# Kernel optimization log

Measured on AMD Instinct MI355X. Metric: run time of the kernel, lower is better.

The kernel has to match this reference:

```python
import jax, jax.numpy as jnp
import numpy as np

NUM_USERS = 100000
NUM_ITEMS = 50000
N_NODES = NUM_USERS + NUM_ITEMS
EMB = 64          # emb_dim == layers[0]
NNZ = 2_400_000   # ~16 avg degree normalized-Laplacian nonzeros
BATCH = 16384


def spmm(rows, cols, vals, x, n):
    # sparse (COO) Laplacian @ dense features: out[r] += v * x[c]
    return jax.ops.segment_sum(vals[:, None] * x[cols], rows, num_segments=n)


def setup_inputs() -> dict:
    key = jax.random.key(0)
    ks = jax.random.split(key, 20)
    userIdx = jax.random.randint(ks[0], (BATCH,), 0, NUM_USERS)
    itemIdx = jax.random.randint(ks[1], (BATCH,), 0, NUM_ITEMS)
    lap_rows = jax.random.randint(ks[2], (NNZ,), 0, N_NODES, dtype=jnp.int32)
    lap_cols = jax.random.randint(ks[3], (NNZ,), 0, N_NODES, dtype=jnp.int32)
    # normalized Laplacian values ~ 1/sqrt(deg_i*deg_j), small positive
    lap_vals = jax.random.uniform(ks[4], (NNZ,), dtype=jnp.float32) * 0.05
    uEmb = jax.random.normal(ks[5], (NUM_USERS, EMB), dtype=jnp.float32) * 0.1
    iEmb = jax.random.normal(ks[6], (NUM_ITEMS, EMB), dtype=jnp.float32) * 0.1
    s = 1.0 / np.sqrt(EMB)
    gW0 = jax.random.normal(ks[7], (EMB, EMB), dtype=jnp.float32) * s
    gb0 = jnp.zeros((EMB,), jnp.float32)
    gW1 = jax.random.normal(ks[8], (EMB, EMB), dtype=jnp.float32) * s
    gb1 = jnp.zeros((EMB,), jnp.float32)
    D_CAT = EMB * 3 * 2  # 384
    W1 = jax.random.normal(ks[9], (D_CAT, 64), dtype=jnp.float32) / np.sqrt(D_CAT)
    b1 = jnp.zeros((64,), jnp.float32)
    W2 = jax.random.normal(ks[10], (64, 32), dtype=jnp.float32) / 8.0
    b2 = jnp.zeros((32,), jnp.float32)
    W3 = jax.random.normal(ks[11], (32, 1), dtype=jnp.float32) / np.sqrt(32.0)
    b3 = jnp.zeros((1,), jnp.float32)
    return {"userIdx": userIdx, "itemIdx": itemIdx,
            "lap_rows": lap_rows, "lap_cols": lap_cols, "lap_vals": lap_vals,
            "uEmb": uEmb, "iEmb": iEmb,
            "gW0": gW0, "gb0": gb0, "gW1": gW1, "gb1": gb1,
            "W1": W1, "b1": b1, "W2": W2, "b2": b2, "W3": W3, "b3": b3}


def reference(userIdx, itemIdx, lap_rows, lap_cols, lap_vals,
              uEmb, iEmb, gW0, gb0, gW1, gb1, W1, b1, W2, b2, W3, b3):
    features = jnp.concatenate([uEmb, iEmb], axis=0)  # [N, EMB]
    final = features
    for W, b in ((gW0, gb0), (gW1, gb1)):
        # (Laplacian + selfLoop I) @ features, then linear + ReLU
        h = spmm(lap_rows, lap_cols, lap_vals, features, N_NODES) + features
        features = jax.nn.relu(h @ W + b)
        final = jnp.concatenate([final, features], axis=1)
    u = final[userIdx]                     # [B, 192]
    it = final[itemIdx + NUM_USERS]        # [B, 192]
    e = jnp.concatenate([u, it], axis=1)   # [B, 384]
    e = jax.nn.relu(e @ W1 + b1)
    e = e @ W2 + b2
    e = e @ W3 + b3
    return e.ravel()
```

## Files before the change

### kernel.cpp

```cpp
#include <hip/hip_runtime.h>
#include <hip/hip_bf16.h>

#define NUM_USERS 100000
#define NUM_ITEMS 50000
#define N_NODES   150000
#define EMB       64
#define NNZ       2400000
#define BATCH     16384
#define D_CAT     384
#define BSHIFT    8
#define NBUCK     ((N_NODES + 255) >> 8)
#define EPB       9375

__device__ __forceinline__ unsigned short f2bf(float f) {
    unsigned u = __float_as_uint(f);
    unsigned r = u + 0x7fffu + ((u >> 16) & 1u);
    return (unsigned short)(r >> 16);
}
__device__ __forceinline__ float bflo(unsigned u) { return __uint_as_float(u << 16); }
__device__ __forceinline__ float bfhi(unsigned u) { return __uint_as_float(u & 0xffff0000u); }

__global__ __launch_bounds__(1024) void bucket_hist(const int* __restrict__ rows,
                                                    int* __restrict__ bcnt, int nnz) {
    __shared__ int h[NBUCK];
    int tid = threadIdx.x;
    for (int i = tid; i < NBUCK; i += 1024) h[i] = 0;
    __syncthreads();
    for (int i = blockIdx.x * 1024 + tid; i < nnz; i += gridDim.x * 1024)
        atomicAdd(&h[rows[i] >> BSHIFT], 1);
    __syncthreads();
    for (int i = tid; i < NBUCK; i += 1024) {
        int c = h[i];
        if (c) atomicAdd(&bcnt[i], c);
    }
}

__global__ __launch_bounds__(1024) void bucket_scan(const int* __restrict__ bcnt,
                                                    int* __restrict__ boffs,
                                                    int* __restrict__ gtails, int nnz) {
    __shared__ int s[1024];
    int t = threadIdx.x;
    int x = (t < NBUCK) ? bcnt[t] : 0;
    s[t] = x;
    __syncthreads();
#pragma unroll
    for (int off = 1; off < 1024; off <<= 1) {
        int v = (t >= off) ? s[t - off] : 0;
        __syncthreads();
        s[t] += v;
        __syncthreads();
    }
    if (t < NBUCK) {
        int e = s[t] - x;
        boffs[t] = e;
        gtails[t] = e;
    }
    if (t == 0) boffs[NBUCK] = nnz;
}

__global__ __launch_bounds__(1024) void coarse_multisplit(const int* __restrict__ rows,
                                                          const int* __restrict__ cols,
                                                          const float* __restrict__ vals,
                                                          int* __restrict__ gtails,
                                                          int2* __restrict__ pv, int nnz) {
    extern __shared__ int dyn[];
    int2* stage = (int2*)dyn;
    int*  smap  = dyn + 2 * EPB;
    __shared__ int hcnt[NBUCK];
    __shared__ int lstart[NBUCK];
    __shared__ int shiftv[NBUCK];

    int tid = threadIdx.x;
    int e0 = blockIdx.x * EPB;
    int e1 = e0 + EPB < nnz ? e0 + EPB : nnz;
    int nE = e1 - e0;

    for (int i = tid; i < NBUCK; i += 1024) hcnt[i] = 0;
    __syncthreads();
    for (int i = e0 + tid; i < e1; i += 1024)
        atomicAdd(&hcnt[rows[i] >> BSHIFT], 1);
    __syncthreads();

    int cnt = (tid < NBUCK) ? hcnt[tid] : 0;
    smap[tid] = cnt;
    __syncthreads();
#pragma unroll
    for (int off = 1; off < 1024; off <<= 1) {
        int v = (tid >= off) ? smap[tid - off] : 0;
        __syncthreads();
        smap[tid] += v;
        __syncthreads();
    }
    if (tid < NBUCK) {
        int ls = smap[tid] - cnt;
        lstart[tid] = ls;
        hcnt[tid] = ls;
        int gb = cnt ? atomicAdd(&gtails[tid], cnt) : 0;
        shiftv[tid] = gb - ls;
    }
    __syncthreads();

    for (int b = tid; b < NBUCK; b += 1024) {
        int beg = lstart[b];
        int end_ = (b == NBUCK - 1) ? nE : lstart[b + 1];
        int sh = shiftv[b];
        for (int k = beg; k < end_; ++k) smap[k] = sh;
    }
    __syncthreads();

    for (int i = e0 + tid; i < e1; i += 1024) {
        int r = rows[i];
        int p = atomicAdd(&hcnt[r >> BSHIFT], 1);
        stage[p] = make_int2(((r & 255) << 18) | cols[i], __float_as_int(vals[i]));
    }
    __syncthreads();

    for (int j = tid; j < nE; j += 1024)
        pv[smap[j] + j] = stage[j];
}

__global__ __launch_bounds__(1024) void fine_scatter(const int* __restrict__ boffs,
                                                     const int2* __restrict__ pv,
                                                     int2* __restrict__ packed,
                                                     int* __restrict__ row_ptr, int nnz) {
    __shared__ int rcnt[256];
    __shared__ int loff[256];
    int b = blockIdx.x;
    int tid = threadIdx.x;
    int lo = boffs[b], hi = boffs[b + 1];
    int r0 = b << BSHIFT;
    int nr = N_NODES - r0; if (nr > 256) nr = 256;

    if (tid < 256) rcnt[tid] = 0;
    __syncthreads();
    for (int i = lo + tid; i < hi; i += 1024)
        atomicAdd(&rcnt[pv[i].x >> 18], 1);
    __syncthreads();
    if (tid < 256) loff[tid] = rcnt[tid];
    __syncthreads();
#pragma unroll
    for (int off = 1; off < 256; off <<= 1) {
        int v = (tid < 256 && tid >= off) ? loff[tid - off] : 0;
        __syncthreads();
        if (tid < 256) loff[tid] += v;
        __syncthreads();
    }
    if (tid < 256) {
        int e = lo + loff[tid] - rcnt[tid];
        loff[tid] = e;
        if (tid < nr) row_ptr[r0 + tid] = e;
    }
    if (b == 0 && tid == 0) row_ptr[N_NODES] = nnz;
    __syncthreads();
    for (int i = lo + tid; i < hi; i += 1024) {
        int2 e = pv[i];
        int rl = e.x >> 18;
        int pos = atomicAdd(&loff[rl], 1);
        packed[pos] = make_int2(e.x & 0x3FFFF, e.y);
    }
}

__global__ __launch_bounds__(256) void gemm_table_f32(const float* __restrict__ uE,
                                                      const float* __restrict__ iE,
                                                      const float* __restrict__ W,
                                                      unsigned short* __restrict__ Zh,
                                                      int n_rows) {
    __shared__ float Wl[64 * 64];
    __shared__ float Xf[64 * 64];
    int tid = threadIdx.x;
    int lane = tid & 63;
    int wave = tid >> 6;
    int r0 = blockIdx.x * 64;
    int last = n_rows - 1;

    for (int i = tid; i < 64 * 64; i += 256) Wl[i] = W[i];
    for (int i = tid; i < 64 * 16; i += 256) {
        int row = i >> 4, q = i & 15;
        int r = r0 + row; r = r > last ? last : r;
        const float4* src = (r < NUM_USERS)
            ? (const float4*)(uE + (size_t)r * 64)
            : (const float4*)(iE + (size_t)(r - NUM_USERS) * 64);
        ((float4*)Xf)[i] = src[q];
    }
    __syncthreads();

    int rbase = wave * 16;
    float acc[16];
#pragma unroll
    for (int i = 0; i < 16; ++i) acc[i] = 0.f;

#pragma unroll 1
    for (int kc = 0; kc < 16; ++kc) {
        float w0 = Wl[(kc * 4 + 0) * 64 + lane];
        float w1 = Wl[(kc * 4 + 1) * 64 + lane];
        float w2 = Wl[(kc * 4 + 2) * 64 + lane];
        float w3 = Wl[(kc * 4 + 3) * 64 + lane];
#pragma unroll
        for (int i = 0; i < 16; ++i) {
            float4 q = ((const float4*)Xf)[(rbase + i) * 16 + kc];
            acc[i] = fmaf(q.x, w0, acc[i]);
            acc[i] = fmaf(q.y, w1, acc[i]);
            acc[i] = fmaf(q.z, w2, acc[i]);
            acc[i] = fmaf(q.w, w3, acc[i]);
        }
    }
#pragma unroll
    for (int i = 0; i < 16; ++i) {
        int r = r0 + rbase + i;
        if (r < n_rows) Zh[(size_t)r * 64 + lane] = f2bf(acc[i]);
    }
}

__global__ __launch_bounds__(256) void gemm_table_bf16(const unsigned* __restrict__ Xh,
                                                       const float* __restrict__ W,
                                                       unsigned short* __restrict__ Zh,
                                                       int n_rows) {
    __shared__ float Wl[64 * 64];
    __shared__ uint4 Xl4[64 * 8];
    int tid = threadIdx.x;
    int lane = tid & 63;
    int wave = tid >> 6;
    int r0 = blockIdx.x * 64;
    int nr = n_rows - r0; if (nr > 64) nr = 64;

    for (int i = tid; i < 64 * 64; i += 256) Wl[i] = W[i];
    const uint4* Xg4 = (const uint4*)(Xh + (size_t)r0 * 32);
    for (int i = tid; i < nr * 8; i += 256) Xl4[i] = Xg4[i];
    __syncthreads();

    const unsigned* Xl = (const unsigned*)Xl4;
    int rbase = wave * 16;
    float acc[16];
#pragma unroll
    for (int i = 0; i < 16; ++i) acc[i] = 0.f;

#pragma unroll 1
    for (int kc = 0; kc < 8; ++kc) {
        float w0 = Wl[(kc * 8 + 0) * 64 + lane];
        float w1 = Wl[(kc * 8 + 1) * 64 + lane];
        float w2 = Wl[(kc * 8 + 2) * 64 + lane];
        float w3 = Wl[(kc * 8 + 3) * 64 + lane];
        float w4 = Wl[(kc * 8 + 4) * 64 + lane];
        float w5 = Wl[(kc * 8 + 5) * 64 + lane];
        float w6 = Wl[(kc * 8 + 6) * 64 + lane];
        float w7 = Wl[(kc * 8 + 7) * 64 + lane];
#pragma unroll
        for (int i = 0; i < 16; ++i) {
            uint4 q = *(const uint4*)&Xl[(rbase + i) * 32 + kc * 4];
            acc[i] = fmaf(bflo(q.x), w0, acc[i]);
            acc[i] = fmaf(bfhi(q.x), w1, acc[i]);
            acc[i] = fmaf(bflo(q.y), w2, acc[i]);
            acc[i] = fmaf(bfhi(q.y), w3, acc[i]);
            acc[i] = fmaf(bflo(q.z), w4, acc[i]);
            acc[i] = fmaf(bfhi(q.z), w5, acc[i]);
            acc[i] = fmaf(bflo(q.w), w6, acc[i]);
            acc[i] = fmaf(bfhi(q.w), w7, acc[i]);
        }
    }
#pragma unroll
    for (int i = 0; i < 16; ++i) {
        int r = r0 + rbase + i;
        if (r < n_rows) Zh[(size_t)r * 64 + lane] = f2bf(acc[i]);
    }
}

__global__ __launch_bounds__(256) void spmm_bias_relu(const int* __restrict__ row_ptr,
                                                      const int2* __restrict__ packed,
                                                      const uint2* __restrict__ zh2,
                                                      const float* __restrict__ bias,
                                                      uint2* __restrict__ outh2,
                                                      int n_rows) {
    int tid = threadIdx.x;
    int lane = tid & 63;
    int wave = tid >> 6;
    int q = lane >> 4;
    int k = lane & 15;
    int r = blockIdx.x * 4 + wave;
    if (r >= n_rows) return;

    uint2 su = zh2[(size_t)r * 16 + k];
    float4 acc;
    acc.x = q ? 0.f : bflo(su.x);
    acc.y = q ? 0.f : bfhi(su.x);
    acc.z = q ? 0.f : bflo(su.y);
    acc.w = q ? 0.f : bfhi(su.y);

    int e = row_ptr[r] + q;
    int end = row_ptr[r + 1];
    for (; e + 13 < end; e += 16) {
        int2 p0 = packed[e + 0];
        int2 p1 = packed[e + 4];
        int2 p2 = packed[e + 8];
        int2 p3 = packed[e + 12];
        uint2 z0 = zh2[(size_t)p0.x * 16 + k];
        uint2 z1 = zh2[(size_t)p1.x * 16 + k];
        uint2 z2 = zh2[(size_t)p2.x * 16 + k];
        uint2 z3 = zh2[(size_t)p3.x * 16 + k];
        float v0 = __int_as_float(p0.y), v1 = __int_as_float(p1.y);
        float v2 = __int_as_float(p2.y), v3 = __int_as_float(p3.y);
        acc.x = fmaf(v0, bflo(z0.x), acc.x); acc.y = fmaf(v0, bfhi(z0.x), acc.y);
        acc.z = fmaf(v0, bflo(z0.y), acc.z); acc.w = fmaf(v0, bfhi(z0.y), acc.w);
        acc.x = fmaf(v1, bflo(z1.x), acc.x); acc.y = fmaf(v1, bfhi(z1.x), acc.y);
        acc.z = fmaf(v1, bflo(z1.y), acc.z); acc.w = fmaf(v1, bfhi(z1.y), acc.w);
        acc.x = fmaf(v2, bflo(z2.x), acc.x); acc.y = fmaf(v2, bfhi(z2.x), acc.y);
        acc.z = fmaf(v2, bflo(z2.y), acc.z); acc.w = fmaf(v2, bfhi(z2.y), acc.w);
        acc.x = fmaf(v3, bflo(z3.x), acc.x); acc.y = fmaf(v3, bfhi(z3.x), acc.y);
        acc.z = fmaf(v3, bflo(z3.y), acc.z); acc.w = fmaf(v3, bfhi(z3.y), acc.w);
    }
    for (; e < end; e += 4) {
        int2 p = packed[e];
        uint2 z = zh2[(size_t)p.x * 16 + k];
        float v = __int_as_float(p.y);
        acc.x = fmaf(v, bflo(z.x), acc.x); acc.y = fmaf(v, bfhi(z.x), acc.y);
        acc.z = fmaf(v, bflo(z.y), acc.z); acc.w = fmaf(v, bfhi(z.y), acc.w);
    }

    acc.x += __shfl_xor(acc.x, 16, 64);
    acc.y += __shfl_xor(acc.y, 16, 64);
    acc.z += __shfl_xor(acc.z, 16, 64);
    acc.w += __shfl_xor(acc.w, 16, 64);
    acc.x += __shfl_xor(acc.x, 32, 64);
    acc.y += __shfl_xor(acc.y, 32, 64);
    acc.z += __shfl_xor(acc.z, 32, 64);
    acc.w += __shfl_xor(acc.w, 32, 64);
    if (q == 0) {
        float4 bv = ((const float4*)bias)[k];
        float a = fmaxf(acc.x + bv.x, 0.f);
        float b = fmaxf(acc.y + bv.y, 0.f);
        float c = fmaxf(acc.z + bv.z, 0.f);
        float d = fmaxf(acc.w + bv.w, 0.f);
        outh2[(size_t)r * 16 + k] = make_uint2(
            ((unsigned)f2bf(b) << 16) | (unsigned)f2bf(a),
            ((unsigned)f2bf(d) << 16) | (unsigned)f2bf(c));
    }
}

__global__ __launch_bounds__(1024) void fused_mlp(
        const int* __restrict__ userIdx, const int* __restrict__ itemIdx,
        const float* __restrict__ uEmb, const float* __restrict__ iEmb,
        const unsigned short* __restrict__ feat1h,
        const unsigned short* __restrict__ feat2h,
        const float* __restrict__ W1, const float* __restrict__ b1,
        const float* __restrict__ W2, const float* __restrict__ b2,
        const float* __restrict__ W3, const float* __restrict__ b3,
        float* __restrict__ out) {
    __shared__ float    Wl[128 * 64];
    __shared__ unsigned El[64 * 64];
    __shared__ float    Ht[64 * 64];
    __shared__ float    W2l[64 * 32];
    __shared__ float    w3l[32];
    __shared__ float    b2l[32];
    __shared__ int      uidx[64], iidx[64];
    int tid = threadIdx.x;
    int lane = tid & 63;
    int wave = tid >> 6;
    int r0 = blockIdx.x * 64;
    int rbase = wave * 4;

    if (tid < 64) uidx[tid] = userIdx[r0 + tid];
    else if (tid < 128) iidx[tid - 64] = itemIdx[r0 + tid - 64];
    if (tid < 32) { w3l[tid] = W3[tid]; b2l[tid] = b2[tid]; }
    for (int i = tid; i < 64 * 32; i += 1024) W2l[i] = W2[i];

    float acc[4];
    float bv = b1[lane];
#pragma unroll
    for (int i = 0; i < 4; ++i) acc[i] = bv;

#pragma unroll 1
    for (int c = 0; c < 3; ++c) {
        __syncthreads();
        for (int i = tid; i < 128 * 64; i += 1024) Wl[i] = W1[c * 128 * 64 + i];
        {
            int t = tid;
            int row = t >> 4;
            int seg = (t >> 3) & 1;
            int q   = t & 7;
            int gseg = c * 2 + seg;
            uint4 val;
            if (gseg == 0 || gseg == 3) {
                const float* p = (gseg == 0)
                    ? uEmb + (size_t)uidx[row] * 64 + q * 8
                    : iEmb + (size_t)iidx[row] * 64 + q * 8;
                float4 a = *(const float4*)p;
                float4 b = *(const float4*)(p + 4);
                val.x = ((unsigned)f2bf(a.y) << 16) | f2bf(a.x);
                val.y = ((unsigned)f2bf(a.w) << 16) | f2bf(a.z);
                val.z = ((unsigned)f2bf(b.y) << 16) | f2bf(b.x);
                val.w = ((unsigned)f2bf(b.w) << 16) | f2bf(b.z);
            } else {
                const unsigned short* src;
                if (gseg == 1)      src = feat1h + (size_t)uidx[row] * 64;
                else if (gseg == 2) src = feat2h + (size_t)uidx[row] * 64;
                else if (gseg == 4) src = feat1h + (size_t)(iidx[row] + NUM_USERS) * 64;
                else                src = feat2h + (size_t)(iidx[row] + NUM_USERS) * 64;
                val = *(const uint4*)(src + q * 8);
            }
            *(uint4*)&El[row * 64 + seg * 32 + q * 4] = val;
        }
        __syncthreads();
        const uint4* El4 = (const uint4*)El;
#pragma unroll 1
        for (int k = 0; k < 128; k += 8) {
            float w0 = Wl[(k + 0) * 64 + lane];
            float w1 = Wl[(k + 1) * 64 + lane];
            float w2 = Wl[(k + 2) * 64 + lane];
            float w3 = Wl[(k + 3) * 64 + lane];
            float w4 = Wl[(k + 4) * 64 + lane];
            float w5 = Wl[(k + 5) * 64 + lane];
            float w6 = Wl[(k + 6) * 64 + lane];
            float w7 = Wl[(k + 7) * 64 + lane];
#pragma unroll
            for (int i = 0; i < 4; ++i) {
                uint4 q = El4[(rbase + i) * 16 + (k >> 3)];
                acc[i] = fmaf(bflo(q.x), w0, acc[i]);
                acc[i] = fmaf(bfhi(q.x), w1, acc[i]);
                acc[i] = fmaf(bflo(q.y), w2, acc[i]);
                acc[i] = fmaf(bfhi(q.y), w3, acc[i]);
                acc[i] = fmaf(bflo(q.z), w4, acc[i]);
                acc[i] = fmaf(bfhi(q.z), w5, acc[i]);
                acc[i] = fmaf(bflo(q.w), w6, acc[i]);
                acc[i] = fmaf(bfhi(q.w), w7, acc[i]);
            }
        }
    }

#pragma unroll
    for (int i = 0; i < 4; ++i) Ht[(rbase + i) * 64 + lane] = fmaxf(acc[i], 0.f);
    __syncthreads();

    int half = lane >> 5;
    int k = lane & 31;
    float b3v = b3[0];
#pragma unroll 1
    for (int p = 0; p < 2; ++p) {
        int row = rbase + p * 2 + half;
        float z = b2l[k];
#pragma unroll
        for (int j = 0; j < 64; ++j)
            z = fmaf(Ht[row * 64 + j], W2l[j * 32 + k], z);
        z *= w3l[k];
#pragma unroll
        for (int off = 16; off; off >>= 1)
            z += __shfl_xor(z, off, 64);
        if (k == 0) out[r0 + row] = z + b3v;
    }
}

extern "C" void kernel_launch(void* const* d_in, const int* in_sizes, int n_in,
                              void* d_out, int out_size, void* d_ws, size_t ws_size,
                              hipStream_t stream) {
    const int*   userIdx = (const int*)  d_in[0];
    const int*   itemIdx = (const int*)  d_in[1];
    const int*   lap_rows= (const int*)  d_in[2];
    const int*   lap_cols= (const int*)  d_in[3];
    const float* lap_vals= (const float*)d_in[4];
    const float* uEmb    = (const float*)d_in[5];
    const float* iEmb    = (const float*)d_in[6];
    const float* gW0     = (const float*)d_in[7];
    const float* gb0     = (const float*)d_in[8];
    const float* gW1     = (const float*)d_in[9];
    const float* gb1     = (const float*)d_in[10];
    const float* W1      = (const float*)d_in[11];
    const float* b1      = (const float*)d_in[12];
    const float* W2      = (const float*)d_in[13];
    const float* b2      = (const float*)d_in[14];
    const float* W3      = (const float*)d_in[15];
    const float* b3      = (const float*)d_in[16];
    float* out = (float*)d_out;

    const size_t NF = (size_t)N_NODES * EMB;
    char* w = (char*)d_ws;
    unsigned short* bufA = (unsigned short*)w;
    unsigned short* bufB = bufA + NF;
    char*  region3 = (char*)(bufB + NF);
    int2*  pv      = (int2*)region3;
    unsigned short* Zh = (unsigned short*)region3;
    int2*  packed  = (int2*)(region3 + NF * sizeof(float));
    int*   row_ptr = (int*)(packed + NNZ);
    int*   boffs   = row_ptr + (N_NODES + 1);
    int*   gtails  = boffs + (NBUCK + 1);
    int*   bcnt    = gtails + NBUCK;

    const int ms_grid   = (NNZ + EPB - 1) / EPB;
    const int ms_lds    = EPB * 12;
    const int spmm_grid = (N_NODES + 3) / 4;
    const int gemm_grid = (N_NODES + 63) / 64;

    hipMemsetAsync(bcnt, 0, NBUCK * sizeof(int), stream);
    bucket_hist<<<256, 1024, 0, stream>>>(lap_rows, bcnt, NNZ);
    bucket_scan<<<1, 1024, 0, stream>>>(bcnt, boffs, gtails, NNZ);
    coarse_multisplit<<<ms_grid, 1024, ms_lds, stream>>>(lap_rows, lap_cols, lap_vals,
                                                         gtails, pv, NNZ);
    fine_scatter<<<NBUCK, 1024, 0, stream>>>(boffs, pv, packed, row_ptr, NNZ);

    gemm_table_f32<<<gemm_grid, 256, 0, stream>>>(uEmb, iEmb, gW0, Zh, N_NODES);
    spmm_bias_relu<<<spmm_grid, 256, 0, stream>>>(row_ptr, packed, (const uint2*)Zh,
                                                  gb0, (uint2*)bufA, N_NODES);

    gemm_table_bf16<<<gemm_grid, 256, 0, stream>>>((const unsigned*)bufA, gW1, Zh, N_NODES);
    spmm_bias_relu<<<spmm_grid, 256, 0, stream>>>(row_ptr, packed, (const uint2*)Zh,
                                                  gb1, (uint2*)bufB, N_NODES);

    fused_mlp<<<BATCH / 64, 1024, 0, stream>>>(userIdx, itemIdx, uEmb, iEmb,
                                               bufA, bufB, W1, b1, W2, b2, W3, b3, out);
}
```

Before: 456.7 us.

## Fuse CSR build into one persistent kernel with grid barriers

Merges the histogram, scan, coarse multisplit and fine scatter kernels into a single persistent kernel of 256 blocks. Software grid barriers replace the kernel boundaries, and the fine scatter stage pulls buckets from an atomic task queue. Each block caches its rows in LDS so the rows array is read only once. The aim is to remove launch gaps and the redundant first histogram pass. The risk is deadlock if the 256 blocks of 1024 threads with about 112KB of LDS cannot all be resident together, plus barrier spin overhead.

```diff
diff --git a/kernel.cpp b/kernel.cpp
--- a/kernel.cpp
+++ b/kernel.cpp
@@ -10,7 +10,8 @@
 #define D_CAT     384
 #define BSHIFT    8
 #define NBUCK     ((N_NODES + 255) >> 8)
-#define EPB       9375
+#define CSR_GRID  256
+#define EPB       (NNZ / CSR_GRID)
 
 __device__ __forceinline__ unsigned short f2bf(float f) {
     unsigned u = __float_as_uint(f);
@@ -20,143 +21,145 @@
 __device__ __forceinline__ float bflo(unsigned u) { return __uint_as_float(u << 16); }
 __device__ __forceinline__ float bfhi(unsigned u) { return __uint_as_float(u & 0xffff0000u); }
 
-__global__ __launch_bounds__(1024) void bucket_hist(const int* __restrict__ rows,
-                                                    int* __restrict__ bcnt, int nnz) {
-    __shared__ int h[NBUCK];
-    int tid = threadIdx.x;
-    for (int i = tid; i < NBUCK; i += 1024) h[i] = 0;
-    __syncthreads();
-    for (int i = blockIdx.x * 1024 + tid; i < nnz; i += gridDim.x * 1024)
-        atomicAdd(&h[rows[i] >> BSHIFT], 1);
-    __syncthreads();
-    for (int i = tid; i < NBUCK; i += 1024) {
-        int c = h[i];
-        if (c) atomicAdd(&bcnt[i], c);
-    }
-}
-
-__global__ __launch_bounds__(1024) void bucket_scan(const int* __restrict__ bcnt,
-                                                    int* __restrict__ boffs,
-                                                    int* __restrict__ gtails, int nnz) {
-    __shared__ int s[1024];
-    int t = threadIdx.x;
-    int x = (t < NBUCK) ? bcnt[t] : 0;
-    s[t] = x;
-    __syncthreads();
-#pragma unroll
-    for (int off = 1; off < 1024; off <<= 1) {
-        int v = (t >= off) ? s[t - off] : 0;
-        __syncthreads();
-        s[t] += v;
-        __syncthreads();
-    }
-    if (t < NBUCK) {
-        int e = s[t] - x;
-        boffs[t] = e;
-        gtails[t] = e;
-    }
-    if (t == 0) boffs[NBUCK] = nnz;
-}
-
-__global__ __launch_bounds__(1024) void coarse_multisplit(const int* __restrict__ rows,
-                                                          const int* __restrict__ cols,
-                                                          const float* __restrict__ vals,
-                                                          int* __restrict__ gtails,
-                                                          int2* __restrict__ pv, int nnz) {
+__device__ __forceinline__ void grid_barrier(int* bar, int nblk) {
+    __syncthreads();
+    if (threadIdx.x == 0) {
+        __threadfence();
+        atomicAdd(bar, 1);
+        while (__hip_atomic_load(bar, __ATOMIC_RELAXED, __HIP_MEMORY_SCOPE_AGENT) < nblk)
+            __builtin_amdgcn_s_sleep(2);
+        __threadfence();
+    }
+    __syncthreads();
+}
+
+__global__ __launch_bounds__(1024) void csr_build(const int* __restrict__ rows,
+                                                  const int* __restrict__ cols,
+                                                  const float* __restrict__ vals,
+                                                  int* __restrict__ aux,
+                                                  int2* __restrict__ pv,
+                                                  int2* __restrict__ packed,
+                                                  int* __restrict__ row_ptr) {
     extern __shared__ int dyn[];
     int2* stage = (int2*)dyn;
     int*  smap  = dyn + 2 * EPB;
     __shared__ int hcnt[NBUCK];
-    __shared__ int lstart[NBUCK];
-    __shared__ int shiftv[NBUCK];
+    __shared__ int lst[NBUCK];
+    __shared__ int shf[NBUCK];
+    __shared__ int lbo[NBUCK + 1];
+    __shared__ int scn[1024];
+    __shared__ int rcnt[256], loff[256];
+    __shared__ int tsk;
+
+    int* gtails2 = aux;
+    int* bcnt    = aux + NBUCK;
+    int* taskc   = aux + 2 * NBUCK;
+    int* bar     = aux + 2 * NBUCK + 1;
 
     int tid = threadIdx.x;
     int e0 = blockIdx.x * EPB;
-    int e1 = e0 + EPB < nnz ? e0 + EPB : nnz;
-    int nE = e1 - e0;
+    const int nE = EPB;
 
     for (int i = tid; i < NBUCK; i += 1024) hcnt[i] = 0;
     __syncthreads();
-    for (int i = e0 + tid; i < e1; i += 1024)
-        atomicAdd(&hcnt[rows[i] >> BSHIFT], 1);
+    for (int i = tid; i < nE; i += 1024) {
+        int r = rows[e0 + i];
+        smap[i] = r;
+        atomicAdd(&hcnt[r >> BSHIFT], 1);
+    }
+    __syncthreads();
+    for (int i = tid; i < NBUCK; i += 1024) {
+        int c = hcnt[i];
+        if (c) atomicAdd(&bcnt[i], c);
+    }
+    grid_barrier(bar, CSR_GRID);
+
+    int x = (tid < NBUCK) ? bcnt[tid] : 0;
+    scn[tid] = x;
+    __syncthreads();
+#pragma unroll
+    for (int off = 1; off < 1024; off <<= 1) {
+        int v = (tid >= off) ? scn[tid - off] : 0;
+        __syncthreads();
+        scn[tid] += v;
+        __syncthreads();
+    }
+    if (tid < NBUCK) lbo[tid] = scn[tid] - x;
+    if (tid == 0) lbo[NBUCK] = NNZ;
     __syncthreads();
 
     int cnt = (tid < NBUCK) ? hcnt[tid] : 0;
-    smap[tid] = cnt;
+    scn[tid] = cnt;
     __syncthreads();
 #pragma unroll
     for (int off = 1; off < 1024; off <<= 1) {
-        int v = (tid >= off) ? smap[tid - off] : 0;
-        __syncthreads();
-        smap[tid] += v;
+        int v = (tid >= off) ? scn[tid - off] : 0;
+        __syncthreads();
+        scn[tid] += v;
         __syncthreads();
     }
     if (tid < NBUCK) {
-        int ls = smap[tid] - cnt;
-        lstart[tid] = ls;
+        int ls = scn[tid] - cnt;
+        lst[tid] = ls;
         hcnt[tid] = ls;
-        int gb = cnt ? atomicAdd(&gtails[tid], cnt) : 0;
-        shiftv[tid] = gb - ls;
-    }
-    __syncthreads();
-
+        int gb = cnt ? (lbo[tid] + atomicAdd(&gtails2[tid], cnt)) : 0;
+        shf[tid] = gb - ls;
+    }
+    __syncthreads();
+    for (int i = tid; i < nE; i += 1024) {
+        int r = smap[i];
+        int p = atomicAdd(&hcnt[r >> BSHIFT], 1);
+        stage[p] = make_int2(((r & 255) << 18) | cols[e0 + i], __float_as_int(vals[e0 + i]));
+    }
+    __syncthreads();
     for (int b = tid; b < NBUCK; b += 1024) {
-        int beg = lstart[b];
-        int end_ = (b == NBUCK - 1) ? nE : lstart[b + 1];
-        int sh = shiftv[b];
+        int beg = lst[b];
+        int end_ = (b == NBUCK - 1) ? nE : lst[b + 1];
+        int sh = shf[b];
         for (int k = beg; k < end_; ++k) smap[k] = sh;
     }
     __syncthreads();
-
-    for (int i = e0 + tid; i < e1; i += 1024) {
-        int r = rows[i];
-        int p = atomicAdd(&hcnt[r >> BSHIFT], 1);
-        stage[p] = make_int2(((r & 255) << 18) | cols[i], __float_as_int(vals[i]));
-    }
-    __syncthreads();
-
     for (int j = tid; j < nE; j += 1024)
         pv[smap[j] + j] = stage[j];
-}
-
-__global__ __launch_bounds__(1024) void fine_scatter(const int* __restrict__ boffs,
-                                                     const int2* __restrict__ pv,
-                                                     int2* __restrict__ packed,
-                                                     int* __restrict__ row_ptr, int nnz) {
-    __shared__ int rcnt[256];
-    __shared__ int loff[256];
-    int b = blockIdx.x;
-    int tid = threadIdx.x;
-    int lo = boffs[b], hi = boffs[b + 1];
-    int r0 = b << BSHIFT;
-    int nr = N_NODES - r0; if (nr > 256) nr = 256;
-
-    if (tid < 256) rcnt[tid] = 0;
-    __syncthreads();
-    for (int i = lo + tid; i < hi; i += 1024)
-        atomicAdd(&rcnt[pv[i].x >> 18], 1);
-    __syncthreads();
-    if (tid < 256) loff[tid] = rcnt[tid];
-    __syncthreads();
-#pragma unroll
-    for (int off = 1; off < 256; off <<= 1) {
-        int v = (tid < 256 && tid >= off) ? loff[tid - off] : 0;
-        __syncthreads();
-        if (tid < 256) loff[tid] += v;
-        __syncthreads();
-    }
-    if (tid < 256) {
-        int e = lo + loff[tid] - rcnt[tid];
-        loff[tid] = e;
-        if (tid < nr) row_ptr[r0 + tid] = e;
-    }
-    if (b == 0 && tid == 0) row_ptr[N_NODES] = nnz;
-    __syncthreads();
-    for (int i = lo + tid; i < hi; i += 1024) {
-        int2 e = pv[i];
-        int rl = e.x >> 18;
-        int pos = atomicAdd(&loff[rl], 1);
-        packed[pos] = make_int2(e.x & 0x3FFFF, e.y);
+    grid_barrier(bar + 1, CSR_GRID);
+
+    for (;;) {
+        __syncthreads();
+        if (tid == 0) tsk = atomicAdd(taskc, 1);
+        __syncthreads();
+        int b = tsk;
+        if (b >= NBUCK) break;
+        int lo = lbo[b], hi = lbo[b + 1];
+        int r0 = b << BSHIFT;
+        int nr = N_NODES - r0; if (nr > 256) nr = 256;
+
+        if (tid < 256) rcnt[tid] = 0;
+        __syncthreads();
+        for (int i = lo + tid; i < hi; i += 1024)
+            atomicAdd(&rcnt[pv[i].x >> 18], 1);
+        __syncthreads();
+        if (tid < 256) loff[tid] = rcnt[tid];
+        __syncthreads();
+#pragma unroll
+        for (int off = 1; off < 256; off <<= 1) {
+            int v = (tid < 256 && tid >= off) ? loff[tid - off] : 0;
+            __syncthreads();
+            if (tid < 256) loff[tid] += v;
+            __syncthreads();
+        }
+        if (tid < 256) {
+            int e = lo + loff[tid] - rcnt[tid];
+            loff[tid] = e;
+            if (tid < nr) row_ptr[r0 + tid] = e;
+        }
+        if (b == 0 && tid == 0) row_ptr[N_NODES] = NNZ;
+        __syncthreads();
+        for (int i = lo + tid; i < hi; i += 1024) {
+            int2 e = pv[i];
+            int rl = e.x >> 18;
+            int pos = atomicAdd(&loff[rl], 1);
+            packed[pos] = make_int2(e.x & 0x3FFFF, e.y);
+        }
     }
 }
 
@@ -478,21 +481,15 @@
     unsigned short* Zh = (unsigned short*)region3;
     int2*  packed  = (int2*)(region3 + NF * sizeof(float));
     int*   row_ptr = (int*)(packed + NNZ);
-    int*   boffs   = row_ptr + (N_NODES + 1);
-    int*   gtails  = boffs + (NBUCK + 1);
-    int*   bcnt    = gtails + NBUCK;
-
-    const int ms_grid   = (NNZ + EPB - 1) / EPB;
-    const int ms_lds    = EPB * 12;
+    int*   aux     = row_ptr + (N_NODES + 1);
+
+    const int csr_lds   = EPB * 12;
     const int spmm_grid = (N_NODES + 3) / 4;
     const int gemm_grid = (N_NODES + 63) / 64;
 
-    hipMemsetAsync(bcnt, 0, NBUCK * sizeof(int), stream);
-    bucket_hist<<<256, 1024, 0, stream>>>(lap_rows, bcnt, NNZ);
-    bucket_scan<<<1, 1024, 0, stream>>>(bcnt, boffs, gtails, NNZ);
-    coarse_multisplit<<<ms_grid, 1024, ms_lds, stream>>>(lap_rows, lap_cols, lap_vals,
-                                                         gtails, pv, NNZ);
-    fine_scatter<<<NBUCK, 1024, 0, stream>>>(boffs, pv, packed, row_ptr, NNZ);
+    hipMemsetAsync(aux, 0, (2 * NBUCK + 8) * sizeof(int), stream);
+    csr_build<<<CSR_GRID, 1024, csr_lds, stream>>>(lap_rows, lap_cols, lap_vals,
+                                                   aux, pv, packed, row_ptr);
 
     gemm_table_f32<<<gemm_grid, 256, 0, stream>>>(uEmb, iEmb, gW0, Zh, N_NODES);
     spmm_bias_relu<<<spmm_grid, 256, 0, stream>>>(row_ptr, packed, (const uint2*)Zh,
```

New measurement: 504.3 us. 1.1x slower.

## Fuse second-layer dense transform into first SpMM epilogue

Applied to the files above, without the earlier changes.

The first SpMM kernel now also multiplies each finished output row by gW1, staged in shared memory, and writes the transformed bf16 row into a separate workspace buffer. This removes the separate gemm_table_bf16 launch and its re-read of bufA. Each SpMM block now loads a 16KB weight tile and does 64 extra FMAs per lane, which adds LDS traffic and occupancy pressure to a memory-bound gather kernel. A fallback keeps the old path when the workspace is too small.

```diff
diff --git a/kernel.cpp b/kernel.cpp
--- a/kernel.cpp
+++ b/kernel.cpp
@@ -264,18 +264,27 @@
     }
 }
 
+template<int FZ>
 __global__ __launch_bounds__(256) void spmm_bias_relu(const int* __restrict__ row_ptr,
                                                       const int2* __restrict__ packed,
                                                       const uint2* __restrict__ zh2,
                                                       const float* __restrict__ bias,
                                                       uint2* __restrict__ outh2,
+                                                      const float* __restrict__ Wz,
+                                                      unsigned short* __restrict__ Zh_out,
                                                       int n_rows) {
+    extern __shared__ float Wl[];
     int tid = threadIdx.x;
     int lane = tid & 63;
     int wave = tid >> 6;
     int q = lane >> 4;
     int k = lane & 15;
     int r = blockIdx.x * 4 + wave;
+
+    if constexpr (FZ) {
+        for (int i = tid; i < 64 * 64; i += 256) Wl[i] = Wz[i];
+        __syncthreads();
+    }
     if (r >= n_rows) return;
 
     uint2 su = zh2[(size_t)r * 16 + k];
@@ -323,15 +332,29 @@
     acc.y += __shfl_xor(acc.y, 32, 64);
     acc.z += __shfl_xor(acc.z, 32, 64);
     acc.w += __shfl_xor(acc.w, 32, 64);
-    if (q == 0) {
-        float4 bv = ((const float4*)bias)[k];
-        float a = fmaxf(acc.x + bv.x, 0.f);
-        float b = fmaxf(acc.y + bv.y, 0.f);
-        float c = fmaxf(acc.z + bv.z, 0.f);
-        float d = fmaxf(acc.w + bv.w, 0.f);
-        outh2[(size_t)r * 16 + k] = make_uint2(
-            ((unsigned)f2bf(b) << 16) | (unsigned)f2bf(a),
-            ((unsigned)f2bf(d) << 16) | (unsigned)f2bf(c));
+
+    float4 bv = ((const float4*)bias)[k];
+    float a = fmaxf(acc.x + bv.x, 0.f);
+    float b = fmaxf(acc.y + bv.y, 0.f);
+    float c = fmaxf(acc.z + bv.z, 0.f);
+    float d = fmaxf(acc.w + bv.w, 0.f);
+    unsigned pa = ((unsigned)f2bf(b) << 16) | (unsigned)f2bf(a);
+    unsigned pb = ((unsigned)f2bf(d) << 16) | (unsigned)f2bf(c);
+    if (q == 0)
+        outh2[(size_t)r * 16 + k] = make_uint2(pa, pb);
+
+    if constexpr (FZ) {
+        float z = 0.f;
+#pragma unroll
+        for (int jj = 0; jj < 16; ++jj) {
+            unsigned u0 = __shfl(pa, jj, 64);
+            unsigned u1 = __shfl(pb, jj, 64);
+            z = fmaf(bflo(u0), Wl[(4 * jj + 0) * 64 + lane], z);
+            z = fmaf(bfhi(u0), Wl[(4 * jj + 1) * 64 + lane], z);
+            z = fmaf(bflo(u1), Wl[(4 * jj + 2) * 64 + lane], z);
+            z = fmaf(bfhi(u1), Wl[(4 * jj + 3) * 64 + lane], z);
+        }
+        Zh_out[(size_t)r * 64 + lane] = f2bf(z);
     }
 }
 
@@ -481,6 +504,9 @@
     int*   boffs   = row_ptr + (N_NODES + 1);
     int*   gtails  = boffs + (NBUCK + 1);
     int*   bcnt    = gtails + NBUCK;
+    size_t tail_off = ((size_t)((char*)(bcnt + NBUCK) - w) + 15) & ~(size_t)15;
+    unsigned short* Zh2 = (unsigned short*)(w + tail_off);
+    bool fuse = (tail_off + NF * sizeof(unsigned short)) <= ws_size;
 
     const int ms_grid   = (NNZ + EPB - 1) / EPB;
     const int ms_lds    = EPB * 12;
@@ -495,12 +521,20 @@
     fine_scatter<<<NBUCK, 1024, 0, stream>>>(boffs, pv, packed, row_ptr, NNZ);
 
     gemm_table_f32<<<gemm_grid, 256, 0, stream>>>(uEmb, iEmb, gW0, Zh, N_NODES);
-    spmm_bias_relu<<<spmm_grid, 256, 0, stream>>>(row_ptr, packed, (const uint2*)Zh,
-                                                  gb0, (uint2*)bufA, N_NODES);
-
-    gemm_table_bf16<<<gemm_grid, 256, 0, stream>>>((const unsigned*)bufA, gW1, Zh, N_NODES);
-    spmm_bias_relu<<<spmm_grid, 256, 0, stream>>>(row_ptr, packed, (const uint2*)Zh,
-                                                  gb1, (uint2*)bufB, N_NODES);
+
+    if (fuse) {
+        spmm_bias_relu<1><<<spmm_grid, 256, 16384, stream>>>(row_ptr, packed,
+            (const uint2*)Zh, gb0, (uint2*)bufA, gW1, Zh2, N_NODES);
+        spmm_bias_relu<0><<<spmm_grid, 256, 0, stream>>>(row_ptr, packed,
+            (const uint2*)Zh2, gb1, (uint2*)bufB, nullptr, nullptr, N_NODES);
+    } else {
+        spmm_bias_relu<0><<<spmm_grid, 256, 0, stream>>>(row_ptr, packed,
+            (const uint2*)Zh, gb0, (uint2*)bufA, nullptr, nullptr, N_NODES);
+        gemm_table_bf16<<<gemm_grid, 256, 0, stream>>>((const unsigned*)bufA, gW1,
+                                                       Zh, N_NODES);
+        spmm_bias_relu<0><<<spmm_grid, 256, 0, stream>>>(row_ptr, packed,
+            (const uint2*)Zh, gb1, (uint2*)bufB, nullptr, nullptr, N_NODES);
+    }
 
     fused_mlp<<<BATCH / 64, 1024, 0, stream>>>(userIdx, itemIdx, uEmb, iEmb,
                                                bufA, bufB, W1, b1, W2, b2, W3, b3, out);
```

New measurement: 499.4 us. 9.4% more time.

## Keep weight columns in registers and stream rows via scalar loads in table GEMMs

Applied to the files above, without the earlier changes.

Both dense table GEMM kernels drop their LDS staging of weights and input rows. Each lane now keeps its 64-entry weight column in VGPRs, and each wave reads one row at a time with s_load_dwordx4 into SGPRs, which broadcasts the row to all lanes. This removes LDS traffic and the block barrier. In exchange, each row waits serially on scalar loads with a full lgkmcnt(0), VGPR pressure rises, and each wave computes one row at a time with less ILP.

```diff
diff --git a/kernel.cpp b/kernel.cpp
--- a/kernel.cpp
+++ b/kernel.cpp
@@ -12,6 +12,8 @@
 #define NBUCK     ((N_NODES + 255) >> 8)
 #define EPB       9375
 
+typedef int si4 __attribute__((ext_vector_type(4)));
+
 __device__ __forceinline__ unsigned short f2bf(float f) {
     unsigned u = __float_as_uint(f);
     unsigned r = u + 0x7fffu + ((u >> 16) & 1u);
@@ -19,6 +21,13 @@
 }
 __device__ __forceinline__ float bflo(unsigned u) { return __uint_as_float(u << 16); }
 __device__ __forceinline__ float bfhi(unsigned u) { return __uint_as_float(u & 0xffff0000u); }
+
+__device__ __forceinline__ const void* rfl_ptr(const void* p) {
+    unsigned long long u = (unsigned long long)p;
+    unsigned lo = __builtin_amdgcn_readfirstlane((unsigned)u);
+    unsigned hi = __builtin_amdgcn_readfirstlane((unsigned)(u >> 32));
+    return (const void*)((((unsigned long long)hi) << 32) | lo);
+}
 
 __global__ __launch_bounds__(1024) void bucket_hist(const int* __restrict__ rows,
                                                     int* __restrict__ bcnt, int nnz) {
@@ -165,102 +174,110 @@
                                                       const float* __restrict__ W,
                                                       unsigned short* __restrict__ Zh,
                                                       int n_rows) {
-    __shared__ float Wl[64 * 64];
-    __shared__ float Xf[64 * 64];
     int tid = threadIdx.x;
     int lane = tid & 63;
     int wave = tid >> 6;
-    int r0 = blockIdx.x * 64;
+    int r0 = blockIdx.x * 64 + wave * 16;
     int last = n_rows - 1;
 
-    for (int i = tid; i < 64 * 64; i += 256) Wl[i] = W[i];
-    for (int i = tid; i < 64 * 16; i += 256) {
-        int row = i >> 4, q = i & 15;
-        int r = r0 + row; r = r > last ? last : r;
-        const float4* src = (r < NUM_USERS)
-            ? (const float4*)(uE + (size_t)r * 64)
-            : (const float4*)(iE + (size_t)(r - NUM_USERS) * 64);
-        ((float4*)Xf)[i] = src[q];
-    }
-    __syncthreads();
-
-    int rbase = wave * 16;
-    float acc[16];
-#pragma unroll
-    for (int i = 0; i < 16; ++i) acc[i] = 0.f;
+    float wreg[64];
+#pragma unroll
+    for (int k = 0; k < 64; ++k) wreg[k] = W[k * 64 + lane];
 
 #pragma unroll 1
-    for (int kc = 0; kc < 16; ++kc) {
-        float w0 = Wl[(kc * 4 + 0) * 64 + lane];
-        float w1 = Wl[(kc * 4 + 1) * 64 + lane];
-        float w2 = Wl[(kc * 4 + 2) * 64 + lane];
-        float w3 = Wl[(kc * 4 + 3) * 64 + lane];
-#pragma unroll
-        for (int i = 0; i < 16; ++i) {
-            float4 q = ((const float4*)Xf)[(rbase + i) * 16 + kc];
-            acc[i] = fmaf(q.x, w0, acc[i]);
-            acc[i] = fmaf(q.y, w1, acc[i]);
-            acc[i] = fmaf(q.z, w2, acc[i]);
-            acc[i] = fmaf(q.w, w3, acc[i]);
-        }
-    }
-#pragma unroll
     for (int i = 0; i < 16; ++i) {
-        int r = r0 + rbase + i;
-        if (r < n_rows) Zh[(size_t)r * 64 + lane] = f2bf(acc[i]);
-    }
-}
-
-__global__ __launch_bounds__(256) void gemm_table_bf16(const unsigned* __restrict__ Xh,
+        int r = r0 + i;
+        int rl = r > last ? last : r;
+        const float* xp = (const float*)rfl_ptr(
+            (rl < NUM_USERS) ? (const void*)(uE + (size_t)rl * 64)
+                             : (const void*)(iE + (size_t)(rl - NUM_USERS) * 64));
+        float acc = 0.f;
+        si4 x0, x1, x2, x3, x4, x5, x6, x7;
+        asm volatile(
+            "s_load_dwordx4 %0, %8, 0x0\n\t"
+            "s_load_dwordx4 %1, %8, 0x10\n\t"
+            "s_load_dwordx4 %2, %8, 0x20\n\t"
+            "s_load_dwordx4 %3, %8, 0x30\n\t"
+            "s_load_dwordx4 %4, %8, 0x40\n\t"
+            "s_load_dwordx4 %5, %8, 0x50\n\t"
+            "s_load_dwordx4 %6, %8, 0x60\n\t"
+            "s_load_dwordx4 %7, %8, 0x70"
+            : "=&s"(x0), "=&s"(x1), "=&s"(x2), "=&s"(x3),
+              "=&s"(x4), "=&s"(x5), "=&s"(x6), "=&s"(x7)
+            : "s"(xp));
+        asm volatile("s_waitcnt lgkmcnt(0)" ::: "memory");
+        __builtin_amdgcn_sched_barrier(0);
+#define F4(B, K)  acc = fmaf(__int_as_float((B).x), wreg[(K) + 0], acc); \
+                  acc = fmaf(__int_as_float((B).y), wreg[(K) + 1], acc); \
+                  acc = fmaf(__int_as_float((B).z), wreg[(K) + 2], acc); \
+                  acc = fmaf(__int_as_float((B).w), wreg[(K) + 3], acc);
+        F4(x0, 0)  F4(x1, 4)  F4(x2, 8)  F4(x3, 12)
+        F4(x4, 16) F4(x5, 20) F4(x6, 24) F4(x7, 28)
+        asm volatile(
+            "s_load_dwordx4 %0, %8, 0x80\n\t"
+            "s_load_dwordx4 %1, %8, 0x90\n\t"
+            "s_load_dwordx4 %2, %8, 0xa0\n\t"
+            "s_load_dwordx4 %3, %8, 0xb0\n\t"
+            "s_load_dwordx4 %4, %8, 0xc0\n\t"
+            "s_load_dwordx4 %5, %8, 0xd0\n\t"
+            "s_load_dwordx4 %6, %8, 0xe0\n\t"
+            "s_load_dwordx4 %7, %8, 0xf0"
+            : "=&s"(x0), "=&s"(x1), "=&s"(x2), "=&s"(x3),
+              "=&s"(x4), "=&s"(x5), "=&s"(x6), "=&s"(x7)
+            : "s"(xp));
+        asm volatile("s_waitcnt lgkmcnt(0)" ::: "memory");
+        __builtin_amdgcn_sched_barrier(0);
+        F4(x0, 32) F4(x1, 36) F4(x2, 40) F4(x3, 44)
+        F4(x4, 48) F4(x5, 52) F4(x6, 56) F4(x7, 60)
+#undef F4
+        if (r < n_rows) Zh[(size_t)r * 64 + lane] = f2bf(acc);
+    }
+}
+
+__global__ __launch_bounds__(256) void gemm_table_bf16(const unsigned short* __restrict__ Xh,
                                                        const float* __restrict__ W,
                                                        unsigned short* __restrict__ Zh,
                                                        int n_rows) {
-    __shared__ float Wl[64 * 64];
-    __shared__ uint4 Xl4[64 * 8];
     int tid = threadIdx.x;
     int lane = tid & 63;
     int wave = tid >> 6;
-    int r0 = blockIdx.x * 64;
-    int nr = n_rows - r0; if (nr > 64) nr = 64;
-
-    for (int i = tid; i < 64 * 64; i += 256) Wl[i] = W[i];
-    const uint4* Xg4 = (const uint4*)(Xh + (size_t)r0 * 32);
-    for (int i = tid; i < nr * 8; i += 256) Xl4[i] = Xg4[i];
-    __syncthreads();
-
-    const unsigned* Xl = (const unsigned*)Xl4;
-    int rbase = wave * 16;
-    float acc[16];
-#pragma unroll
-    for (int i = 0; i < 16; ++i) acc[i] = 0.f;
+    int r0 = blockIdx.x * 64 + wave * 16;
+    int last = n_rows - 1;
+
+    float wreg[64];
+#pragma unroll
+    for (int k = 0; k < 64; ++k) wreg[k] = W[k * 64 + lane];
 
 #pragma unroll 1
-    for (int kc = 0; kc < 8; ++kc) {
-        float w0 = Wl[(kc * 8 + 0) * 64 + lane];
-        float w1 = Wl[(kc * 8 + 1) * 64 + lane];
-        float w2 = Wl[(kc * 8 + 2) * 64 + lane];
-        float w3 = Wl[(kc * 8 + 3) * 64 + lane];
-        float w4 = Wl[(kc * 8 + 4) * 64 + lane];
-        float w5 = Wl[(kc * 8 + 5) * 64 + lane];
-        float w6 = Wl[(kc * 8 + 6) * 64 + lane];
-        float w7 = Wl[(kc * 8 + 7) * 64 + lane];
-#pragma unroll
-        for (int i = 0; i < 16; ++i) {
-            uint4 q = *(const uint4*)&Xl[(rbase + i) * 32 + kc * 4];
-            acc[i] = fmaf(bflo(q.x), w0, acc[i]);
-            acc[i] = fmaf(bfhi(q.x), w1, acc[i]);
-            acc[i] = fmaf(bflo(q.y), w2, acc[i]);
-            acc[i] = fmaf(bfhi(q.y), w3, acc[i]);
-            acc[i] = fmaf(bflo(q.z), w4, acc[i]);
-            acc[i] = fmaf(bfhi(q.z), w5, acc[i]);
-            acc[i] = fmaf(bflo(q.w), w6, acc[i]);
-            acc[i] = fmaf(bfhi(q.w), w7, acc[i]);
-        }
-    }
-#pragma unroll
     for (int i = 0; i < 16; ++i) {
-        int r = r0 + rbase + i;
-        if (r < n_rows) Zh[(size_t)r * 64 + lane] = f2bf(acc[i]);
+        int r = r0 + i;
+        int rl = r > last ? last : r;
+        const unsigned short* xp =
+            (const unsigned short*)rfl_ptr(Xh + (size_t)rl * 64);
+        float acc = 0.f;
+        si4 x0, x1, x2, x3, x4, x5, x6, x7;
+        asm volatile(
+            "s_load_dwordx4 %0, %8, 0x0\n\t"
+            "s_load_dwordx4 %1, %8, 0x10\n\t"
+            "s_load_dwordx4 %2, %8, 0x20\n\t"
+            "s_load_dwordx4 %3, %8, 0x30\n\t"
+            "s_load_dwordx4 %4, %8, 0x40\n\t"
+            "s_load_dwordx4 %5, %8, 0x50\n\t"
+            "s_load_dwordx4 %6, %8, 0x60\n\t"
+            "s_load_dwordx4 %7, %8, 0x70"
+            : "=&s"(x0), "=&s"(x1), "=&s"(x2), "=&s"(x3),
+              "=&s"(x4), "=&s"(x5), "=&s"(x6), "=&s"(x7)
+            : "s"(xp));
+        asm volatile("s_waitcnt lgkmcnt(0)" ::: "memory");
+        __builtin_amdgcn_sched_barrier(0);
+#define FD(V, K)  acc = fmaf(bflo((unsigned)(V)), wreg[(K) + 0], acc); \
+                  acc = fmaf(bfhi((unsigned)(V)), wreg[(K) + 1], acc);
+#define F8(B, K)  FD((B).x, (K) + 0) FD((B).y, (K) + 2) FD((B).z, (K) + 4) FD((B).w, (K) + 6)
+        F8(x0, 0)  F8(x1, 8)  F8(x2, 16) F8(x3, 24)
+        F8(x4, 32) F8(x5, 40) F8(x6, 48) F8(x7, 56)
+#undef F8
+#undef FD
+        if (r < n_rows) Zh[(size_t)r * 64 + lane] = f2bf(acc);
     }
 }
 
@@ -498,7 +515,7 @@
     spmm_bias_relu<<<spmm_grid, 256, 0, stream>>>(row_ptr, packed, (const uint2*)Zh,
                                                   gb0, (uint2*)bufA, N_NODES);
 
-    gemm_table_bf16<<<gemm_grid, 256, 0, stream>>>((const unsigned*)bufA, gW1, Zh, N_NODES);
+    gemm_table_bf16<<<gemm_grid, 256, 0, stream>>>(bufA, gW1, Zh, N_NODES);
     spmm_bias_relu<<<spmm_grid, 256, 0, stream>>>(row_ptr, packed, (const uint2*)Zh,
                                                   gb1, (uint2*)bufB, N_NODES);
 
```

After: 481.6 us. 1.05x slower.
